# Performance work log

Measured on AMD Instinct MI355X. Metric: run time of the kernel, lower is better.

## Reference

```python
import jax, jax.numpy as jnp
import numpy as np

N_TOKENS = 524288
N_FEATURES = 128
N_MODELS = 16
N_LAYERS = 2


def setup_inputs() -> dict:
    key = jax.random.key(0)
    kx, kw, kb = jax.random.split(key, 3)
    x = jax.random.normal(kx, (N_TOKENS, N_FEATURES), dtype=jnp.float32)
    # per-expert, per-layer Linear weights in torch layout [out, in]
    scale = 1.0 / np.sqrt(N_FEATURES)
    W = jax.random.normal(kw, (N_MODELS, N_LAYERS, N_FEATURES, N_FEATURES), dtype=jnp.float32) * scale
    b = jax.random.normal(kb, (N_MODELS, N_LAYERS, N_FEATURES), dtype=jnp.float32) * scale
    return {"x": x, "W": W, "b": b}


def reference(x, W, b):
    # x: [N, F]; W: [M, L, F_out, F_in]; b: [M, L, F_out]
    # slices = M equal contiguous partitions of the token dim; each slice runs
    # through its own Linear+ReLU stack and is scattered back (here: reshape).
    M, L, Fo, Fi = W.shape
    xs = x.reshape(M, -1, Fi)  # [M, N/M, F] gathered slices
    for l in range(L):  # small fixed depth loop
        xs = jax.nn.relu(jnp.einsum('mnf,mgf->mng', xs, W[:, l]) + b[:, l][:, None, :])
    return xs.reshape(x.shape[0], Fo)
```

## Files before the change

### kernel.cpp

```cpp
#include <hip/hip_runtime.h>


#define NF   128
#define NM   16
#define NTOK 524288
#define TPM  (NTOK / NM)
#define BM   64
#define WPAD 136

typedef __attribute__((ext_vector_type(8))) short bf16x8;
typedef __attribute__((ext_vector_type(4))) float f32x4;

__device__ __forceinline__ unsigned short f2bf(float f) {
    union { float f; unsigned u; } v; v.f = f;
    unsigned r = v.u + 0x7FFFu + ((v.u >> 16) & 1u);
    return (unsigned short)(r >> 16);
}

__global__ __launch_bounds__(256, 2) void mlp16_kernel(
        const float* __restrict__ x, const float* __restrict__ W,
        const float* __restrict__ b, float* __restrict__ out) {
    __shared__ alignas(16) unsigned short sW[NF * WPAD];
    __shared__ alignas(16) unsigned short sY[BM * WPAD];
    __shared__ float sB[2 * NF];

    const int t    = threadIdx.x;
    const int wave = t >> 6;
    const int lane = t & 63;
    const int ln   = lane & 15;
    const int q    = lane >> 4;

    const int m    = blockIdx.x >> 9;
    const int tile = blockIdx.x & 511;
    const int row0 = m * TPM + tile * BM;

    sB[t] = b[m * 2 * NF + t];

    const float4* W0 = (const float4*)(W + (size_t)m * 2 * NF * NF);
    #pragma unroll
    for (int i = 0; i < 16; ++i) {
        int c = t + i * 256;
        float4 w = W0[c];
        unsigned short* d = &sW[(c >> 5) * WPAD + (c & 31) * 4];
        d[0] = f2bf(w.x); d[1] = f2bf(w.y); d[2] = f2bf(w.z); d[3] = f2bf(w.w);
    }
    __syncthreads();

    f32x4 acc[8];
    #pragma unroll
    for (int gt = 0; gt < 8; ++gt) acc[gt] = (f32x4){0.f, 0.f, 0.f, 0.f};

    const float* xrow = x + (size_t)(row0 + wave * 16 + ln) * NF;
    #pragma unroll
    for (int kt = 0; kt < 4; ++kt) {
        const int f0 = kt * 32 + q * 8;
        float4 a0 = *(const float4*)(xrow + f0);
        float4 a1 = *(const float4*)(xrow + f0 + 4);
        bf16x8 af;
        af[0] = (short)f2bf(a0.x); af[1] = (short)f2bf(a0.y);
        af[2] = (short)f2bf(a0.z); af[3] = (short)f2bf(a0.w);
        af[4] = (short)f2bf(a1.x); af[5] = (short)f2bf(a1.y);
        af[6] = (short)f2bf(a1.z); af[7] = (short)f2bf(a1.w);
        #pragma unroll
        for (int gt = 0; gt < 8; ++gt) {
            bf16x8 bfr = *(const bf16x8*)&sW[(gt * 16 + ln) * WPAD + f0];
            acc[gt] = __builtin_amdgcn_mfma_f32_16x16x32_bf16(af, bfr, acc[gt], 0, 0, 0);
        }
    }

    #pragma unroll
    for (int gt = 0; gt < 8; ++gt) {
        const float bias = sB[gt * 16 + ln];
        #pragma unroll
        for (int r = 0; r < 4; ++r) {
            float v = acc[gt][r] + bias;
            v = v > 0.f ? v : 0.f;
            sY[(wave * 16 + q * 4 + r) * WPAD + gt * 16 + ln] = f2bf(v);
        }
    }
    __syncthreads();

    const float4* W1 = W0 + (NF * NF / 4);
    #pragma unroll
    for (int i = 0; i < 16; ++i) {
        int c = t + i * 256;
        float4 w = W1[c];
        unsigned short* d = &sW[(c >> 5) * WPAD + (c & 31) * 4];
        d[0] = f2bf(w.x); d[1] = f2bf(w.y); d[2] = f2bf(w.z); d[3] = f2bf(w.w);
    }
    __syncthreads();

    f32x4 acc2[8];
    #pragma unroll
    for (int gt = 0; gt < 8; ++gt) acc2[gt] = (f32x4){0.f, 0.f, 0.f, 0.f};

    const unsigned short* yrow = &sY[(wave * 16 + ln) * WPAD];
    #pragma unroll
    for (int kt = 0; kt < 4; ++kt) {
        const int f0 = kt * 32 + q * 8;
        bf16x8 af = *(const bf16x8*)(yrow + f0);
        #pragma unroll
        for (int gt = 0; gt < 8; ++gt) {
            bf16x8 bfr = *(const bf16x8*)&sW[(gt * 16 + ln) * WPAD + f0];
            acc2[gt] = __builtin_amdgcn_mfma_f32_16x16x32_bf16(af, bfr, acc2[gt], 0, 0, 0);
        }
    }

    #pragma unroll
    for (int gt = 0; gt < 8; ++gt) {
        const float bias = sB[NF + gt * 16 + ln];
        #pragma unroll
        for (int r = 0; r < 4; ++r) {
            float v = acc2[gt][r] + bias;
            v = v > 0.f ? v : 0.f;
            out[(size_t)(row0 + wave * 16 + q * 4 + r) * NF + gt * 16 + ln] = v;
        }
    }
}

extern "C" void kernel_launch(void* const* d_in, const int* in_sizes, int n_in,
                              void* d_out, int out_size, void* d_ws, size_t ws_size,
                              hipStream_t stream) {
    const float* x = (const float*)d_in[0];
    const float* W = (const float*)d_in[1];
    const float* b = (const float*)d_in[2];
    float* out = (float*)d_out;
    mlp16_kernel<<<dim3(NTOK / BM), dim3(256), 0, stream>>>(x, W, b, out);
}
```

Measured before the change: 470.9 us.

## Pre-convert weights to MFMA fragment layout and stream via global_load_lds

Adds a small pre-kernel that converts all expert weights to bf16 in MFMA-fragment order once per call. The main kernel then loads both layers' weights into LDS using direct global-to-LDS loads instead of per-block fp32 conversion. It also swaps the MFMA operands so outputs are row-contiguous, which allows float4 stores, and doubles the token tile to 128 rows with 512 threads. This removes the redundant per-block weight conversion and the scattered scalar output stores, at the cost of an extra launch and more LDS per block.

```diff
diff --git a/kernel.cpp b/kernel.cpp
--- a/kernel.cpp
+++ b/kernel.cpp
@@ -5,11 +5,14 @@
 #define NM   16
 #define NTOK 524288
 #define TPM  (NTOK / NM)
-#define BM   64
+#define BM   128
+#define BPM  (TPM / BM)
 #define WPAD 136
 
 typedef __attribute__((ext_vector_type(8))) short bf16x8;
+typedef __attribute__((ext_vector_type(4))) short bf16x4v;
 typedef __attribute__((ext_vector_type(4))) float f32x4;
+typedef unsigned int u32;
 
 __device__ __forceinline__ unsigned short f2bf(float f) {
     union { float f; unsigned u; } v; v.f = f;
@@ -17,104 +20,127 @@
     return (unsigned short)(r >> 16);
 }
 
-__global__ __launch_bounds__(256, 2) void mlp16_kernel(
-        const float* __restrict__ x, const float* __restrict__ W,
-        const float* __restrict__ b, float* __restrict__ out) {
-    __shared__ alignas(16) unsigned short sW[NF * WPAD];
-    __shared__ alignas(16) unsigned short sY[BM * WPAD];
-    __shared__ float sB[2 * NF];
+__device__ alignas(16) unsigned short g_Wf[NM * 2 * NF * NF];
+
+__global__ __launch_bounds__(256) void convw_kernel(const float* __restrict__ W) {
+    const int idx  = blockIdx.x * 256 + threadIdx.x;
+    const int lane = idx & 63;
+    const int fid  = (idx >> 6) & 31;
+    const int ml   = idx >> 11;
+    const int row  = (fid >> 2) * 16 + (lane & 15);
+    const int col  = (fid & 3) * 32 + (lane >> 4) * 8;
+    const float* s = W + ((size_t)ml * NF + row) * NF + col;
+    float4 a = *(const float4*)s;
+    float4 c = *(const float4*)(s + 4);
+    unsigned short* d = &g_Wf[(size_t)idx * 8];
+    d[0] = f2bf(a.x); d[1] = f2bf(a.y); d[2] = f2bf(a.z); d[3] = f2bf(a.w);
+    d[4] = f2bf(c.x); d[5] = f2bf(c.y); d[6] = f2bf(c.z); d[7] = f2bf(c.w);
+}
+
+__device__ __forceinline__ void load_lds16(const unsigned short* g, unsigned short* l) {
+    __builtin_amdgcn_global_load_lds(
+        (const __attribute__((address_space(1))) u32*)g,
+        (__attribute__((address_space(3))) u32*)l, 16, 0, 0);
+}
+
+__global__ __launch_bounds__(512, 4) void mlp16_kernel(
+        const float* __restrict__ x, const float* __restrict__ b,
+        float* __restrict__ out) {
+    __shared__ alignas(16) unsigned short buf0[BM * WPAD];
+    __shared__ alignas(16) unsigned short sW1[NF * NF];
+    __shared__ alignas(16) float sB[2 * NF];
 
     const int t    = threadIdx.x;
-    const int wave = t >> 6;
+    const int w    = t >> 6;
     const int lane = t & 63;
     const int ln   = lane & 15;
     const int q    = lane >> 4;
 
-    const int m    = blockIdx.x >> 9;
-    const int tile = blockIdx.x & 511;
+    const int m    = blockIdx.x >> 8;
+    const int tile = blockIdx.x & (BPM - 1);
     const int row0 = m * TPM + tile * BM;
 
-    sB[t] = b[m * 2 * NF + t];
+    if (t < 2 * NF) sB[t] = b[m * 2 * NF + t];
 
-    const float4* W0 = (const float4*)(W + (size_t)m * 2 * NF * NF);
+    const unsigned short* wsrc = g_Wf + (size_t)m * 2 * NF * NF;
     #pragma unroll
-    for (int i = 0; i < 16; ++i) {
-        int c = t + i * 256;
-        float4 w = W0[c];
-        unsigned short* d = &sW[(c >> 5) * WPAD + (c & 31) * 4];
-        d[0] = f2bf(w.x); d[1] = f2bf(w.y); d[2] = f2bf(w.z); d[3] = f2bf(w.w);
+    for (int i = 0; i < 4; ++i) {
+        const int fid = w * 4 + i;
+        load_lds16(wsrc + (size_t)(fid * 64 + lane) * 8, &buf0[fid * 512]);
+        load_lds16(wsrc + NF * NF + (size_t)(fid * 64 + lane) * 8, &sW1[fid * 512]);
     }
+
+    const float* xrow = x + (size_t)(row0 + w * 16 + ln) * NF;
+    float4 xa[8];
+    #pragma unroll
+    for (int kt = 0; kt < 4; ++kt) {
+        xa[2 * kt]     = *(const float4*)(xrow + kt * 32 + q * 8);
+        xa[2 * kt + 1] = *(const float4*)(xrow + kt * 32 + q * 8 + 4);
+    }
+
     __syncthreads();
 
     f32x4 acc[8];
     #pragma unroll
     for (int gt = 0; gt < 8; ++gt) acc[gt] = (f32x4){0.f, 0.f, 0.f, 0.f};
 
-    const float* xrow = x + (size_t)(row0 + wave * 16 + ln) * NF;
     #pragma unroll
     for (int kt = 0; kt < 4; ++kt) {
-        const int f0 = kt * 32 + q * 8;
-        float4 a0 = *(const float4*)(xrow + f0);
-        float4 a1 = *(const float4*)(xrow + f0 + 4);
-        bf16x8 af;
-        af[0] = (short)f2bf(a0.x); af[1] = (short)f2bf(a0.y);
-        af[2] = (short)f2bf(a0.z); af[3] = (short)f2bf(a0.w);
-        af[4] = (short)f2bf(a1.x); af[5] = (short)f2bf(a1.y);
-        af[6] = (short)f2bf(a1.z); af[7] = (short)f2bf(a1.w);
+        const float4 a0 = xa[2 * kt], a1 = xa[2 * kt + 1];
+        bf16x8 xb;
+        xb[0] = (short)f2bf(a0.x); xb[1] = (short)f2bf(a0.y);
+        xb[2] = (short)f2bf(a0.z); xb[3] = (short)f2bf(a0.w);
+        xb[4] = (short)f2bf(a1.x); xb[5] = (short)f2bf(a1.y);
+        xb[6] = (short)f2bf(a1.z); xb[7] = (short)f2bf(a1.w);
         #pragma unroll
         for (int gt = 0; gt < 8; ++gt) {
-            bf16x8 bfr = *(const bf16x8*)&sW[(gt * 16 + ln) * WPAD + f0];
-            acc[gt] = __builtin_amdgcn_mfma_f32_16x16x32_bf16(af, bfr, acc[gt], 0, 0, 0);
+            bf16x8 wf = *(const bf16x8*)&buf0[((gt * 4 + kt) * 64 + lane) * 8];
+            acc[gt] = __builtin_amdgcn_mfma_f32_16x16x32_bf16(wf, xb, acc[gt], 0, 0, 0);
         }
     }
 
+    __syncthreads();
+
     #pragma unroll
     for (int gt = 0; gt < 8; ++gt) {
-        const float bias = sB[gt * 16 + ln];
+        const f32x4 bv = *(const f32x4*)&sB[gt * 16 + q * 4];
+        bf16x4v yv;
         #pragma unroll
         for (int r = 0; r < 4; ++r) {
-            float v = acc[gt][r] + bias;
+            float v = acc[gt][r] + bv[r];
             v = v > 0.f ? v : 0.f;
-            sY[(wave * 16 + q * 4 + r) * WPAD + gt * 16 + ln] = f2bf(v);
+            yv[r] = (short)f2bf(v);
         }
+        *(bf16x4v*)&buf0[(w * 16 + ln) * WPAD + gt * 16 + q * 4] = yv;
     }
-    __syncthreads();
 
-    const float4* W1 = W0 + (NF * NF / 4);
-    #pragma unroll
-    for (int i = 0; i < 16; ++i) {
-        int c = t + i * 256;
-        float4 w = W1[c];
-        unsigned short* d = &sW[(c >> 5) * WPAD + (c & 31) * 4];
-        d[0] = f2bf(w.x); d[1] = f2bf(w.y); d[2] = f2bf(w.z); d[3] = f2bf(w.w);
-    }
     __syncthreads();
 
     f32x4 acc2[8];
     #pragma unroll
     for (int gt = 0; gt < 8; ++gt) acc2[gt] = (f32x4){0.f, 0.f, 0.f, 0.f};
 
-    const unsigned short* yrow = &sY[(wave * 16 + ln) * WPAD];
+    const unsigned short* yrow = &buf0[(w * 16 + ln) * WPAD];
     #pragma unroll
     for (int kt = 0; kt < 4; ++kt) {
-        const int f0 = kt * 32 + q * 8;
-        bf16x8 af = *(const bf16x8*)(yrow + f0);
+        const bf16x8 yb = *(const bf16x8*)(yrow + kt * 32 + q * 8);
         #pragma unroll
         for (int gt = 0; gt < 8; ++gt) {
-            bf16x8 bfr = *(const bf16x8*)&sW[(gt * 16 + ln) * WPAD + f0];
-            acc2[gt] = __builtin_amdgcn_mfma_f32_16x16x32_bf16(af, bfr, acc2[gt], 0, 0, 0);
+            bf16x8 wf = *(const bf16x8*)&sW1[((gt * 4 + kt) * 64 + lane) * 8];
+            acc2[gt] = __builtin_amdgcn_mfma_f32_16x16x32_bf16(wf, yb, acc2[gt], 0, 0, 0);
         }
     }
 
+    float* orow = out + (size_t)(row0 + w * 16 + ln) * NF;
     #pragma unroll
     for (int gt = 0; gt < 8; ++gt) {
-        const float bias = sB[NF + gt * 16 + ln];
-        #pragma unroll
-        for (int r = 0; r < 4; ++r) {
-            float v = acc2[gt][r] + bias;
-            v = v > 0.f ? v : 0.f;
-            out[(size_t)(row0 + wave * 16 + q * 4 + r) * NF + gt * 16 + ln] = v;
-        }
+        const f32x4 bv = *(const f32x4*)&sB[NF + gt * 16 + q * 4];
+        float4 o;
+        float v0 = acc2[gt][0] + bv[0]; o.x = v0 > 0.f ? v0 : 0.f;
+        float v1 = acc2[gt][1] + bv[1]; o.y = v1 > 0.f ? v1 : 0.f;
+        float v2 = acc2[gt][2] + bv[2]; o.z = v2 > 0.f ? v2 : 0.f;
+        float v3 = acc2[gt][3] + bv[3]; o.w = v3 > 0.f ? v3 : 0.f;
+        *(float4*)(orow + gt * 16 + q * 4) = o;
     }
 }
 
@@ -125,5 +151,6 @@
     const float* W = (const float*)d_in[1];
     const float* b = (const float*)d_in[2];
     float* out = (float*)d_out;
-    mlp16_kernel<<<dim3(NTOK / BM), dim3(256), 0, stream>>>(x, W, b, out);
+    convw_kernel<<<dim3(256), dim3(256), 0, stream>>>(W);
+    mlp16_kernel<<<dim3(NTOK / BM), dim3(512), 0, stream>>>(x, b, out);
 }
```

Measured after the change: 441.8 us. -6.2%, faster.
